# Kernel tuning notes

Hardware: AMD Instinct MI355X
Metric: run time of the kernel (lower is better)

Reference implementation:

```python
import jax, jax.numpy as jnp
import numpy as np

HIDDEN = 128
M_DIM = 128
N_NODES = 50000
N_EDGES = 600000

def _linear_params(key, fan_in, fan_out):
    k1, k2 = jax.random.split(key)
    bound = 1.0 / np.sqrt(fan_in)
    W = jax.random.uniform(k1, (fan_in, fan_out), jnp.float32, -bound, bound)
    b = jax.random.uniform(k2, (fan_out,), jnp.float32, -bound, bound)
    return W, b

def setup_inputs() -> dict:
    key = jax.random.key(0)
    ks = jax.random.split(key, 10)
    h = jax.random.normal(ks[0], (N_NODES, HIDDEN), jnp.float32)
    x = jax.random.normal(ks[1], (N_NODES, 3), jnp.float32)
    edge_index = jax.random.randint(ks[2], (2, N_EDGES), 0, N_NODES, jnp.int64)
    We1, be1 = _linear_params(ks[3], 2 * HIDDEN + 1, M_DIM)
    We2, be2 = _linear_params(ks[4], M_DIM, M_DIM)
    Wg, bg = _linear_params(ks[5], M_DIM, 1)
    Wn1, bn1 = _linear_params(ks[6], HIDDEN + M_DIM, HIDDEN)
    Wn2, bn2 = _linear_params(ks[7], HIDDEN, HIDDEN)
    Wc1, bc1 = _linear_params(ks[8], M_DIM, M_DIM)
    Wc2, bc2 = _linear_params(ks[9], M_DIM, 1)
    return {"h": h, "x": x, "edge_index": edge_index,
            "We1": We1, "be1": be1, "We2": We2, "be2": be2,
            "Wg": Wg, "bg": bg,
            "Wn1": Wn1, "bn1": bn1, "Wn2": Wn2, "bn2": bn2,
            "Wc1": Wc1, "bc1": bc1, "Wc2": Wc2, "bc2": bc2}

def reference(h, x, edge_index, We1, be1, We2, be2, Wg, bg,
              Wn1, bn1, Wn2, bn2, Wc1, bc1, Wc2, bc2):
    silu = jax.nn.silu
    row, col = edge_index[0], edge_index[1]
    N = h.shape[0]
    # gather endpoints
    x_j = x[row]          # [E, 3]
    x_i = x[col]          # [E, 3]
    coord_diff = x_i - x_j
    dist = jnp.linalg.norm(coord_diff, axis=-1, keepdims=True)  # [E, 1]
    h_j = h[row]          # [E, H]
    h_i = h[col]          # [E, H]
    msg_inputs = jnp.concatenate([h_i, h_j, dist], axis=-1)     # [E, 2H+1]
    # edge MLP: Linear -> SiLU -> Linear -> SiLU
    m_ij = silu(silu(msg_inputs @ We1 + be1) @ We2 + be2)       # [E, M]
    gate = jax.nn.sigmoid(m_ij @ Wg + bg)                       # [E, 1]
    m_ij = m_ij * gate
    # scatter-add aggregation over destination nodes
    m_aggr = jax.ops.segment_sum(m_ij, col, num_segments=N)     # [N, M]
    node_input = jnp.concatenate([h, m_aggr], axis=-1)          # [N, H+M]
    delta_h = silu(node_input @ Wn1 + bn1) @ Wn2 + bn2
    h_out = h + delta_h
    # coordinate update
    coor_weights = (silu(m_ij @ Wc1 + bc1) @ Wc2 + bc2)         # [E, 1]
    coord_updates = coord_diff * coor_weights                   # [E, 3]
    coord_aggr = jax.ops.segment_sum(coord_updates, col, num_segments=N)
    x_out = x + coord_aggr
    return (h_out, x_out)
```

## Files before the change

### kernel.cpp

```cpp
#include <hip/hip_runtime.h>
#include <cmath>

#define HID 128

typedef __attribute__((ext_vector_type(8))) short bf16x8;
typedef __attribute__((ext_vector_type(4))) float f32x4;

__device__ __forceinline__ unsigned short f2bf(float f) {
    union { float f; unsigned int i; } c; c.f = f;
    unsigned int r = c.i + 0x7fffu + ((c.i >> 16) & 1u);
    return (unsigned short)(r >> 16);
}
__device__ __forceinline__ unsigned cvt_pk(float lo, float hi) {
    unsigned r;
    asm("v_cvt_pk_bf16_f32 %0, %1, %2" : "=v"(r) : "v"(lo), "v"(hi));
    return r;
}
__device__ __forceinline__ float silu_f(float v) {
    float t = __builtin_amdgcn_exp2f(-1.44269504f * v);
    return v * __builtin_amdgcn_rcpf(1.0f + t);
}
__device__ __forceinline__ float sigmoid_f(float v) {
    return __builtin_amdgcn_rcpf(1.0f + __builtin_amdgcn_exp2f(-1.44269504f * v));
}
typedef __fp16 fp16x2 __attribute__((ext_vector_type(2)));
__device__ __forceinline__ void atomic_pk_add_f16(void* p, float lo, float hi) {
    union { fp16x2 h; unsigned u; } cv;
    cv.h = __builtin_amdgcn_cvt_pkrtz(lo, hi);
    unsigned long long a = (unsigned long long)p;
    asm volatile("global_atomic_pk_add_f16 %0, %1, off" :: "v"(a), "v"(cv.u) : "memory");
}

__global__ __launch_bounds__(256) void egnn_prep(
    const float* __restrict__ We1, const float* __restrict__ We2,
    const float* __restrict__ Wc1, const float* __restrict__ Wn1,
    const float* __restrict__ Wn2,
    short* __restrict__ We1p, short* __restrict__ We2p, short* __restrict__ Wc1p,
    short* __restrict__ Wn1p, short* __restrict__ Wn2p)
{
    int t = blockIdx.x * 256 + threadIdx.x;
    int frag = t >> 6, lane = t & 63;
    if (frag >= 224) return;
    const float* W; short* dst; int KC, f;
    if (frag < 64)       { W = We1; dst = We1p; KC = 8; f = frag; }
    else if (frag < 96)  { W = We2; dst = We2p; KC = 4; f = frag - 64; }
    else if (frag < 128) { W = Wc1; dst = Wc1p; KC = 4; f = frag - 96; }
    else if (frag < 192) { W = Wn1; dst = Wn1p; KC = 8; f = frag - 128; }
    else                 { W = Wn2; dst = Wn2p; KC = 4; f = frag - 192; }
    int nt = f / KC, kc = f % KC;
    int n = nt * 16 + (lane & 15);
    short* d = dst + (((size_t)nt * KC + kc) * 64 + lane) * 8;
    #pragma unroll
    for (int j = 0; j < 8; ++j) {
        int k = kc * 32 + ((lane >> 4) << 2) + (j & 3) + ((j >> 2) << 4);
        d[j] = (short)f2bf(W[(size_t)k * HID + n]);
    }
}

__global__ __launch_bounds__(256) void egnn_hpack(
    const float* __restrict__ h, short* __restrict__ h16, int N)
{
    int t = blockIdx.x * 256 + threadIdx.x;
    if (t < N * 32) {
        float4 v = *(const float4*)(h + (size_t)t * 4);
        uint2 p; p.x = cvt_pk(v.x, v.y); p.y = cvt_pk(v.z, v.w);
        *(uint2*)(h16 + (size_t)t * 4) = p;
    }
}

__global__ __launch_bounds__(256) void egnn_edge_mfma(
    const short* __restrict__ h16, const float* __restrict__ x,
    const int* __restrict__ ei, int E,
    const short* __restrict__ We1p, const float* __restrict__ We1,
    const float* __restrict__ be1,
    const short* __restrict__ We2p, const float* __restrict__ be2,
    const float* __restrict__ Wg, const float* __restrict__ bg,
    const short* __restrict__ Wc1p, const float* __restrict__ bc1,
    const float* __restrict__ Wc2, const float* __restrict__ bc2,
    short* __restrict__ m16, float* __restrict__ coord_aggr)
{
    __shared__ short sStage[64 * 256];
    __shared__ float s_be1[128], s_w256[128], s_be2[128];
    __shared__ float s_wg[128], s_bc1[128], s_wc2[128];
    __shared__ int   s_col[64], s_row[64];

    const int tid  = threadIdx.x;
    const int lane = tid & 63;
    const int w    = tid >> 6;
    const int l15  = lane & 15;
    const int g    = lane >> 4;
    const int e0   = blockIdx.x * 64;

    if (tid < 64) {
        s_row[tid] = ei[e0 + tid];
        s_col[tid] = ei[E + e0 + tid];
    }
    if (tid < 128) {
        s_be1[tid]  = be1[tid];
        s_w256[tid] = We1[(size_t)256 * HID + tid];
        s_be2[tid]  = be2[tid];
        s_wg[tid]   = Wg[tid];
        s_bc1[tid]  = bc1[tid];
        s_wc2[tid]  = Wc2[tid];
    }
    __syncthreads();

    #pragma unroll
    for (int it = 0; it < 16; ++it) {
        int e = w + 4 * it;
        int q = lane;
        int node = (q < 32) ? s_col[e] : s_row[e];
        uint2 v = *(const uint2*)(h16 + (size_t)node * HID + (size_t)(q & 31) * 4);
        *(uint2*)((char*)sStage + e * 512 + ((q * 8) ^ ((e & 7) << 4))) = v;
    }

    const int eloc = w * 16 + l15;
    const int nr = s_row[eloc], nc = s_col[eloc];
    float dx = x[nc * 3 + 0] - x[nr * 3 + 0];
    float dy = x[nc * 3 + 1] - x[nr * 3 + 1];
    float dz = x[nc * 3 + 2] - x[nr * 3 + 2];
    float dist = sqrtf(dx * dx + dy * dy + dz * dz);
    __syncthreads();

    const char* stageRow = (const char*)sStage + eloc * 512;
    const int sw = (eloc & 7) << 4;
    const bf16x8* A1 = (const bf16x8*)We1p;
    const bf16x8* A2 = (const bf16x8*)We2p;
    const bf16x8* A3 = (const bf16x8*)Wc1p;

    f32x4 acc[8];
    #pragma unroll
    for (int mt = 0; mt < 8; ++mt) {
        int f = mt * 16 + g * 4;
        #pragma unroll
        for (int r = 0; r < 4; ++r)
            acc[mt][r] = s_be1[f + r] + dist * s_w256[f + r];
    }
    #pragma unroll
    for (int kc = 0; kc < 8; ++kc) {
        int kb = kc * 64 + g * 8;
        uint2 lo = *(const uint2*)(stageRow + ((kb     ) ^ sw));
        uint2 hi = *(const uint2*)(stageRow + ((kb + 32) ^ sw));
        bf16x8 b; ((uint2*)&b)[0] = lo; ((uint2*)&b)[1] = hi;
        #pragma unroll
        for (int mt = 0; mt < 8; ++mt)
            acc[mt] = __builtin_amdgcn_mfma_f32_16x16x32_bf16(A1[(mt * 8 + kc) * 64 + lane], b, acc[mt], 0, 0, 0);
    }

    bf16x8 Bn[4];
    #pragma unroll
    for (int kc = 0; kc < 4; ++kc) {
        unsigned* d = (unsigned*)&Bn[kc];
        d[0] = cvt_pk(silu_f(acc[2 * kc][0]),     silu_f(acc[2 * kc][1]));
        d[1] = cvt_pk(silu_f(acc[2 * kc][2]),     silu_f(acc[2 * kc][3]));
        d[2] = cvt_pk(silu_f(acc[2 * kc + 1][0]), silu_f(acc[2 * kc + 1][1]));
        d[3] = cvt_pk(silu_f(acc[2 * kc + 1][2]), silu_f(acc[2 * kc + 1][3]));
    }

    f32x4 acc2[8];
    #pragma unroll
    for (int mt = 0; mt < 8; ++mt) {
        int f = mt * 16 + g * 4;
        #pragma unroll
        for (int r = 0; r < 4; ++r) acc2[mt][r] = s_be2[f + r];
    }
    #pragma unroll
    for (int kc = 0; kc < 4; ++kc)
        #pragma unroll
        for (int mt = 0; mt < 8; ++mt)
            acc2[mt] = __builtin_amdgcn_mfma_f32_16x16x32_bf16(A2[(mt * 4 + kc) * 64 + lane], Bn[kc], acc2[mt], 0, 0, 0);

    float gp = 0.f;
    #pragma unroll
    for (int mt = 0; mt < 8; ++mt) {
        int f = mt * 16 + g * 4;
        #pragma unroll
        for (int r = 0; r < 4; ++r) {
            float sv = silu_f(acc2[mt][r]);
            acc2[mt][r] = sv;
            gp += sv * s_wg[f + r];
        }
    }
    gp += __shfl_xor(gp, 16, 64);
    gp += __shfl_xor(gp, 32, 64);
    float gate = sigmoid_f(gp + bg[0]);

    #pragma unroll
    for (int mt = 0; mt < 8; ++mt) {
        f32x4 v;
        #pragma unroll
        for (int r = 0; r < 4; ++r) { acc2[mt][r] *= gate; v[r] = acc2[mt][r]; }
        *(f32x4*)((char*)sStage + eloc * 512 + ((g * 16 + mt * 64) ^ sw)) = v;
    }

    bf16x8 B3[4];
    #pragma unroll
    for (int kc = 0; kc < 4; ++kc) {
        unsigned* d = (unsigned*)&B3[kc];
        d[0] = cvt_pk(acc2[2 * kc][0],     acc2[2 * kc][1]);
        d[1] = cvt_pk(acc2[2 * kc][2],     acc2[2 * kc][3]);
        d[2] = cvt_pk(acc2[2 * kc + 1][0], acc2[2 * kc + 1][1]);
        d[3] = cvt_pk(acc2[2 * kc + 1][2], acc2[2 * kc + 1][3]);
    }

    #pragma unroll
    for (int i = 0; i < 16; ++i) {
        int e = w * 16 + i;
        int c = s_col[e];
        int swE = (e & 7) << 4;
        float2 v = *(const float2*)((const char*)sStage + e * 512 + ((lane * 8) ^ swE));
        atomic_pk_add_f16(m16 + (size_t)c * HID + lane * 2, v.x, v.y);
    }

    f32x4 acc3[8];
    #pragma unroll
    for (int mt = 0; mt < 8; ++mt) {
        int f = mt * 16 + g * 4;
        #pragma unroll
        for (int r = 0; r < 4; ++r) acc3[mt][r] = s_bc1[f + r];
    }
    #pragma unroll
    for (int kc = 0; kc < 4; ++kc)
        #pragma unroll
        for (int mt = 0; mt < 8; ++mt)
            acc3[mt] = __builtin_amdgcn_mfma_f32_16x16x32_bf16(A3[(mt * 4 + kc) * 64 + lane], B3[kc], acc3[mt], 0, 0, 0);

    float cwp = 0.f;
    #pragma unroll
    for (int mt = 0; mt < 8; ++mt) {
        int f = mt * 16 + g * 4;
        #pragma unroll
        for (int r = 0; r < 4; ++r)
            cwp += silu_f(acc3[mt][r]) * s_wc2[f + r];
    }
    cwp += __shfl_xor(cwp, 16, 64);
    cwp += __shfl_xor(cwp, 32, 64);
    float cw = cwp + bc2[0];
    if (g == 0) {
        atomicAdd(&coord_aggr[nc * 3 + 0], dx * cw);
        atomicAdd(&coord_aggr[nc * 3 + 1], dy * cw);
        atomicAdd(&coord_aggr[nc * 3 + 2], dz * cw);
    }
}

__global__ __launch_bounds__(256) void egnn_node_mfma(
    const float* __restrict__ h, const float* __restrict__ x,
    const short* __restrict__ m16, const float* __restrict__ coord_aggr,
    const short* __restrict__ Wn1p, const float* __restrict__ bn1,
    const short* __restrict__ Wn2p, const float* __restrict__ bn2,
    float* __restrict__ h_out, float* __restrict__ x_out, int N)
{
    __shared__ short sStage[64 * 256];
    __shared__ float s_bn1[128], s_bn2[128];

    const int tid  = threadIdx.x;
    const int lane = tid & 63;
    const int w    = tid >> 6;
    const int l15  = lane & 15;
    const int g    = lane >> 4;
    const int n0   = blockIdx.x * 64;

    if (tid < 128) { s_bn1[tid] = bn1[tid]; s_bn2[tid] = bn2[tid]; }

    if (tid < 192) {
        int gi = n0 * 3 + tid;
        if (gi < 3 * N) x_out[gi] = x[gi] + coord_aggr[gi];
    }

    #pragma unroll
    for (int it = 0; it < 16; ++it) {
        int e = w + 4 * it;
        int q = lane;
        int node = min(n0 + e, N - 1);
        uint2 pk;
        if (q < 32) {
            float4 v = *(const float4*)&h[(size_t)node * HID + (size_t)q * 4];
            pk.x = cvt_pk(v.x, v.y);
            pk.y = cvt_pk(v.z, v.w);
        } else {
            uint2 hv = *(const uint2*)((const char*)m16 + (size_t)node * 256 + (size_t)(q & 31) * 8);
            const __fp16* hp = (const __fp16*)&hv;
            pk.x = cvt_pk((float)hp[0], (float)hp[1]);
            pk.y = cvt_pk((float)hp[2], (float)hp[3]);
        }
        *(uint2*)((char*)sStage + e * 512 + ((q * 8) ^ ((e & 7) << 4))) = pk;
    }
    __syncthreads();

    const int nloc = w * 16 + l15;
    const int node = n0 + nloc;
    const char* stageRow = (const char*)sStage + nloc * 512;
    const int sw = (nloc & 7) << 4;
    const bf16x8* A1 = (const bf16x8*)Wn1p;
    const bf16x8* A2 = (const bf16x8*)Wn2p;

    f32x4 acc[8];
    #pragma unroll
    for (int mt = 0; mt < 8; ++mt) {
        int f = mt * 16 + g * 4;
        #pragma unroll
        for (int r = 0; r < 4; ++r) acc[mt][r] = s_bn1[f + r];
    }
    #pragma unroll
    for (int kc = 0; kc < 8; ++kc) {
        int kb = kc * 64 + g * 8;
        uint2 lo = *(const uint2*)(stageRow + ((kb     ) ^ sw));
        uint2 hi = *(const uint2*)(stageRow + ((kb + 32) ^ sw));
        bf16x8 b; ((uint2*)&b)[0] = lo; ((uint2*)&b)[1] = hi;
        #pragma unroll
        for (int mt = 0; mt < 8; ++mt)
            acc[mt] = __builtin_amdgcn_mfma_f32_16x16x32_bf16(A1[(mt * 8 + kc) * 64 + lane], b, acc[mt], 0, 0, 0);
    }

    bf16x8 Bn[4];
    #pragma unroll
    for (int kc = 0; kc < 4; ++kc) {
        unsigned* d = (unsigned*)&Bn[kc];
        d[0] = cvt_pk(silu_f(acc[2 * kc][0]),     silu_f(acc[2 * kc][1]));
        d[1] = cvt_pk(silu_f(acc[2 * kc][2]),     silu_f(acc[2 * kc][3]));
        d[2] = cvt_pk(silu_f(acc[2 * kc + 1][0]), silu_f(acc[2 * kc + 1][1]));
        d[3] = cvt_pk(silu_f(acc[2 * kc + 1][2]), silu_f(acc[2 * kc + 1][3]));
    }

    f32x4 acc2[8];
    #pragma unroll
    for (int mt = 0; mt < 8; ++mt) {
        int f = mt * 16 + g * 4;
        #pragma unroll
        for (int r = 0; r < 4; ++r) acc2[mt][r] = s_bn2[f + r];
    }
    #pragma unroll
    for (int kc = 0; kc < 4; ++kc)
        #pragma unroll
        for (int mt = 0; mt < 8; ++mt)
            acc2[mt] = __builtin_amdgcn_mfma_f32_16x16x32_bf16(A2[(mt * 4 + kc) * 64 + lane], Bn[kc], acc2[mt], 0, 0, 0);

    if (node < N) {
        #pragma unroll
        for (int mt = 0; mt < 8; ++mt) {
            size_t base = (size_t)node * HID + mt * 16 + g * 4;
            float4 hres = *(const float4*)&h[base];
            float4 o;
            o.x = acc2[mt][0] + hres.x;
            o.y = acc2[mt][1] + hres.y;
            o.z = acc2[mt][2] + hres.z;
            o.w = acc2[mt][3] + hres.w;
            *(float4*)&h_out[base] = o;
        }
    }
}

extern "C" void kernel_launch(void* const* d_in, const int* in_sizes, int n_in,
                              void* d_out, int out_size, void* d_ws, size_t ws_size,
                              hipStream_t stream) {
    const float* h   = (const float*)d_in[0];
    const float* x   = (const float*)d_in[1];
    const int*   ei  = (const int*)d_in[2];
    const float* We1 = (const float*)d_in[3];
    const float* be1 = (const float*)d_in[4];
    const float* We2 = (const float*)d_in[5];
    const float* be2 = (const float*)d_in[6];
    const float* Wg  = (const float*)d_in[7];
    const float* bg  = (const float*)d_in[8];
    const float* Wn1 = (const float*)d_in[9];
    const float* bn1 = (const float*)d_in[10];
    const float* Wn2 = (const float*)d_in[11];
    const float* bn2 = (const float*)d_in[12];
    const float* Wc1 = (const float*)d_in[13];
    const float* bc1 = (const float*)d_in[14];
    const float* Wc2 = (const float*)d_in[15];
    const float* bc2 = (const float*)d_in[16];

    const int N = in_sizes[0] / HID;
    const int E = in_sizes[2] / 2;

    char* p = (char*)d_ws;
    short* m16        = (short*)p;  p += (size_t)N * 256;
    float* coord_aggr = (float*)p;  p += (size_t)N * 12;
    short* h16        = (short*)p;  p += (size_t)N * 256;
    short* We1p       = (short*)p;  p += 256 * 128 * 2;
    short* We2p       = (short*)p;  p += 128 * 128 * 2;
    short* Wc1p       = (short*)p;  p += 128 * 128 * 2;
    short* Wn1p       = (short*)p;  p += 256 * 128 * 2;
    short* Wn2p       = (short*)p;  p += 128 * 128 * 2;

    (void)hipMemsetAsync(d_ws, 0, (size_t)N * 268, stream);

    float* h_out = (float*)d_out;
    float* x_out = h_out + (size_t)N * HID;

    egnn_prep<<<dim3(56), dim3(256), 0, stream>>>(
        We1, We2, Wc1, Wn1, Wn2, We1p, We2p, Wc1p, Wn1p, Wn2p);
    egnn_hpack<<<dim3((N * 32 + 255) / 256), dim3(256), 0, stream>>>(h, h16, N);
    egnn_edge_mfma<<<dim3((E + 63) / 64), dim3(256), 0, stream>>>(
        h16, x, ei, E, We1p, We1, be1, We2p, be2, Wg, bg, Wc1p, bc1, Wc2, bc2,
        m16, coord_aggr);
    egnn_node_mfma<<<dim3((N + 63) / 64), dim3(256), 0, stream>>>(
        h, x, m16, coord_aggr, Wn1p, bn1, Wn2p, bn2, h_out, x_out, N);
}
```

Before: 378.9 us.

## Split edge MLP into halves and stage messages as packed fp16 in LDS

Each of the three per-edge GEMMs now accumulates 4 output tiles at a time, in two halves, instead of all 8 at once. This roughly halves the live f32 accumulator registers and should allow higher occupancy. The post-SiLU activations are kept as bf16, gated after the reduction, and written to LDS as packed fp16 instead of fp32, so the atomic scatter reads 4-byte words. The trade-offs are extra bf16 rounding of m_ij before gating and scattering, and fewer MFMAs in flight per k-step.

```diff
diff --git a/kernel.cpp b/kernel.cpp
--- a/kernel.cpp
+++ b/kernel.cpp
@@ -16,6 +16,12 @@
     asm("v_cvt_pk_bf16_f32 %0, %1, %2" : "=v"(r) : "v"(lo), "v"(hi));
     return r;
 }
+__device__ __forceinline__ float bflo(unsigned u) {
+    union { unsigned i; float f; } c; c.i = u << 16; return c.f;
+}
+__device__ __forceinline__ float bfhi(unsigned u) {
+    union { unsigned i; float f; } c; c.i = u & 0xffff0000u; return c.f;
+}
 __device__ __forceinline__ float silu_f(float v) {
     float t = __builtin_amdgcn_exp2f(-1.44269504f * v);
     return v * __builtin_amdgcn_rcpf(1.0f + t);
@@ -24,11 +30,14 @@
     return __builtin_amdgcn_rcpf(1.0f + __builtin_amdgcn_exp2f(-1.44269504f * v));
 }
 typedef __fp16 fp16x2 __attribute__((ext_vector_type(2)));
-__device__ __forceinline__ void atomic_pk_add_f16(void* p, float lo, float hi) {
+__device__ __forceinline__ unsigned pkrtz(float lo, float hi) {
     union { fp16x2 h; unsigned u; } cv;
     cv.h = __builtin_amdgcn_cvt_pkrtz(lo, hi);
+    return cv.u;
+}
+__device__ __forceinline__ void atomic_pk_add_f16_raw(void* p, unsigned u) {
     unsigned long long a = (unsigned long long)p;
-    asm volatile("global_atomic_pk_add_f16 %0, %1, off" :: "v"(a), "v"(cv.u) : "memory");
+    asm volatile("global_atomic_pk_add_f16 %0, %1, off" :: "v"(a), "v"(u) : "memory");
 }
 
 __global__ __launch_bounds__(256) void egnn_prep(
@@ -128,79 +137,90 @@
     const bf16x8* A2 = (const bf16x8*)We2p;
     const bf16x8* A3 = (const bf16x8*)Wc1p;
 
-    f32x4 acc[8];
-    #pragma unroll
-    for (int mt = 0; mt < 8; ++mt) {
-        int f = mt * 16 + g * 4;
-        #pragma unroll
-        for (int r = 0; r < 4; ++r)
-            acc[mt][r] = s_be1[f + r] + dist * s_w256[f + r];
-    }
-    #pragma unroll
-    for (int kc = 0; kc < 8; ++kc) {
-        int kb = kc * 64 + g * 8;
-        uint2 lo = *(const uint2*)(stageRow + ((kb     ) ^ sw));
-        uint2 hi = *(const uint2*)(stageRow + ((kb + 32) ^ sw));
-        bf16x8 b; ((uint2*)&b)[0] = lo; ((uint2*)&b)[1] = hi;
-        #pragma unroll
-        for (int mt = 0; mt < 8; ++mt)
-            acc[mt] = __builtin_amdgcn_mfma_f32_16x16x32_bf16(A1[(mt * 8 + kc) * 64 + lane], b, acc[mt], 0, 0, 0);
-    }
-
     bf16x8 Bn[4];
     #pragma unroll
-    for (int kc = 0; kc < 4; ++kc) {
-        unsigned* d = (unsigned*)&Bn[kc];
-        d[0] = cvt_pk(silu_f(acc[2 * kc][0]),     silu_f(acc[2 * kc][1]));
-        d[1] = cvt_pk(silu_f(acc[2 * kc][2]),     silu_f(acc[2 * kc][3]));
-        d[2] = cvt_pk(silu_f(acc[2 * kc + 1][0]), silu_f(acc[2 * kc + 1][1]));
-        d[3] = cvt_pk(silu_f(acc[2 * kc + 1][2]), silu_f(acc[2 * kc + 1][3]));
-    }
-
-    f32x4 acc2[8];
-    #pragma unroll
-    for (int mt = 0; mt < 8; ++mt) {
-        int f = mt * 16 + g * 4;
-        #pragma unroll
-        for (int r = 0; r < 4; ++r) acc2[mt][r] = s_be2[f + r];
-    }
-    #pragma unroll
-    for (int kc = 0; kc < 4; ++kc)
-        #pragma unroll
-        for (int mt = 0; mt < 8; ++mt)
-            acc2[mt] = __builtin_amdgcn_mfma_f32_16x16x32_bf16(A2[(mt * 4 + kc) * 64 + lane], Bn[kc], acc2[mt], 0, 0, 0);
-
+    for (int half = 0; half < 2; ++half) {
+        f32x4 acc[4];
+        #pragma unroll
+        for (int m = 0; m < 4; ++m) {
+            int f = (half * 4 + m) * 16 + g * 4;
+            #pragma unroll
+            for (int r = 0; r < 4; ++r)
+                acc[m][r] = s_be1[f + r] + dist * s_w256[f + r];
+        }
+        #pragma unroll
+        for (int kc = 0; kc < 8; ++kc) {
+            int kb = kc * 64 + g * 8;
+            uint2 lo = *(const uint2*)(stageRow + ((kb     ) ^ sw));
+            uint2 hi = *(const uint2*)(stageRow + ((kb + 32) ^ sw));
+            bf16x8 b; ((uint2*)&b)[0] = lo; ((uint2*)&b)[1] = hi;
+            #pragma unroll
+            for (int m = 0; m < 4; ++m)
+                acc[m] = __builtin_amdgcn_mfma_f32_16x16x32_bf16(
+                    A1[((half * 4 + m) * 8 + kc) * 64 + lane], b, acc[m], 0, 0, 0);
+        }
+        #pragma unroll
+        for (int p = 0; p < 2; ++p) {
+            unsigned* d = (unsigned*)&Bn[half * 2 + p];
+            d[0] = cvt_pk(silu_f(acc[2 * p][0]),     silu_f(acc[2 * p][1]));
+            d[1] = cvt_pk(silu_f(acc[2 * p][2]),     silu_f(acc[2 * p][3]));
+            d[2] = cvt_pk(silu_f(acc[2 * p + 1][0]), silu_f(acc[2 * p + 1][1]));
+            d[3] = cvt_pk(silu_f(acc[2 * p + 1][2]), silu_f(acc[2 * p + 1][3]));
+        }
+    }
+
+    bf16x8 Pn[4];
     float gp = 0.f;
     #pragma unroll
-    for (int mt = 0; mt < 8; ++mt) {
-        int f = mt * 16 + g * 4;
-        #pragma unroll
-        for (int r = 0; r < 4; ++r) {
-            float sv = silu_f(acc2[mt][r]);
-            acc2[mt][r] = sv;
-            gp += sv * s_wg[f + r];
+    for (int half = 0; half < 2; ++half) {
+        f32x4 acc[4];
+        #pragma unroll
+        for (int m = 0; m < 4; ++m) {
+            int f = (half * 4 + m) * 16 + g * 4;
+            #pragma unroll
+            for (int r = 0; r < 4; ++r) acc[m][r] = s_be2[f + r];
+        }
+        #pragma unroll
+        for (int kc = 0; kc < 4; ++kc)
+            #pragma unroll
+            for (int m = 0; m < 4; ++m)
+                acc[m] = __builtin_amdgcn_mfma_f32_16x16x32_bf16(
+                    A2[((half * 4 + m) * 4 + kc) * 64 + lane], Bn[kc], acc[m], 0, 0, 0);
+        #pragma unroll
+        for (int m = 0; m < 4; ++m) {
+            int f = (half * 4 + m) * 16 + g * 4;
+            #pragma unroll
+            for (int r = 0; r < 4; ++r) {
+                float sv = silu_f(acc[m][r]);
+                acc[m][r] = sv;
+                gp += sv * s_wg[f + r];
+            }
+        }
+        #pragma unroll
+        for (int p = 0; p < 2; ++p) {
+            unsigned* d = (unsigned*)&Pn[half * 2 + p];
+            d[0] = cvt_pk(acc[2 * p][0],     acc[2 * p][1]);
+            d[1] = cvt_pk(acc[2 * p][2],     acc[2 * p][3]);
+            d[2] = cvt_pk(acc[2 * p + 1][0], acc[2 * p + 1][1]);
+            d[3] = cvt_pk(acc[2 * p + 1][2], acc[2 * p + 1][3]);
         }
     }
     gp += __shfl_xor(gp, 16, 64);
     gp += __shfl_xor(gp, 32, 64);
     float gate = sigmoid_f(gp + bg[0]);
 
-    #pragma unroll
-    for (int mt = 0; mt < 8; ++mt) {
-        f32x4 v;
-        #pragma unroll
-        for (int r = 0; r < 4; ++r) { acc2[mt][r] *= gate; v[r] = acc2[mt][r]; }
-        *(f32x4*)((char*)sStage + eloc * 512 + ((g * 16 + mt * 64) ^ sw)) = v;
-    }
-
     bf16x8 B3[4];
     #pragma unroll
     for (int kc = 0; kc < 4; ++kc) {
+        const unsigned* s = (const unsigned*)&Pn[kc];
         unsigned* d = (unsigned*)&B3[kc];
-        d[0] = cvt_pk(acc2[2 * kc][0],     acc2[2 * kc][1]);
-        d[1] = cvt_pk(acc2[2 * kc][2],     acc2[2 * kc][3]);
-        d[2] = cvt_pk(acc2[2 * kc + 1][0], acc2[2 * kc + 1][1]);
-        d[3] = cvt_pk(acc2[2 * kc + 1][2], acc2[2 * kc + 1][3]);
+        uint2 w0, w1;
+        { float lo = bflo(s[0]) * gate, hi = bfhi(s[0]) * gate; d[0] = cvt_pk(lo, hi); w0.x = pkrtz(lo, hi); }
+        { float lo = bflo(s[1]) * gate, hi = bfhi(s[1]) * gate; d[1] = cvt_pk(lo, hi); w0.y = pkrtz(lo, hi); }
+        { float lo = bflo(s[2]) * gate, hi = bfhi(s[2]) * gate; d[2] = cvt_pk(lo, hi); w1.x = pkrtz(lo, hi); }
+        { float lo = bflo(s[3]) * gate, hi = bfhi(s[3]) * gate; d[3] = cvt_pk(lo, hi); w1.y = pkrtz(lo, hi); }
+        *(uint2*)((char*)sStage + eloc * 512 + (((2 * kc) * 32 + g * 8) ^ sw))     = w0;
+        *(uint2*)((char*)sStage + eloc * 512 + (((2 * kc + 1) * 32 + g * 8) ^ sw)) = w1;
     }
 
     #pragma unroll
@@ -208,30 +228,33 @@
         int e = w * 16 + i;
         int c = s_col[e];
         int swE = (e & 7) << 4;
-        float2 v = *(const float2*)((const char*)sStage + e * 512 + ((lane * 8) ^ swE));
-        atomic_pk_add_f16(m16 + (size_t)c * HID + lane * 2, v.x, v.y);
-    }
-
-    f32x4 acc3[8];
-    #pragma unroll
-    for (int mt = 0; mt < 8; ++mt) {
-        int f = mt * 16 + g * 4;
-        #pragma unroll
-        for (int r = 0; r < 4; ++r) acc3[mt][r] = s_bc1[f + r];
-    }
-    #pragma unroll
-    for (int kc = 0; kc < 4; ++kc)
-        #pragma unroll
-        for (int mt = 0; mt < 8; ++mt)
-            acc3[mt] = __builtin_amdgcn_mfma_f32_16x16x32_bf16(A3[(mt * 4 + kc) * 64 + lane], B3[kc], acc3[mt], 0, 0, 0);
+        unsigned v = *(const unsigned*)((const char*)sStage + e * 512 + ((lane * 4) ^ swE));
+        atomic_pk_add_f16_raw(m16 + (size_t)c * HID + lane * 2, v);
+    }
 
     float cwp = 0.f;
     #pragma unroll
-    for (int mt = 0; mt < 8; ++mt) {
-        int f = mt * 16 + g * 4;
-        #pragma unroll
-        for (int r = 0; r < 4; ++r)
-            cwp += silu_f(acc3[mt][r]) * s_wc2[f + r];
+    for (int half = 0; half < 2; ++half) {
+        f32x4 acc[4];
+        #pragma unroll
+        for (int m = 0; m < 4; ++m) {
+            int f = (half * 4 + m) * 16 + g * 4;
+            #pragma unroll
+            for (int r = 0; r < 4; ++r) acc[m][r] = s_bc1[f + r];
+        }
+        #pragma unroll
+        for (int kc = 0; kc < 4; ++kc)
+            #pragma unroll
+            for (int m = 0; m < 4; ++m)
+                acc[m] = __builtin_amdgcn_mfma_f32_16x16x32_bf16(
+                    A3[((half * 4 + m) * 4 + kc) * 64 + lane], B3[kc], acc[m], 0, 0, 0);
+        #pragma unroll
+        for (int m = 0; m < 4; ++m) {
+            int f = (half * 4 + m) * 16 + g * 4;
+            #pragma unroll
+            for (int r = 0; r < 4; ++r)
+                cwp += silu_f(acc[m][r]) * s_wc2[f + r];
+        }
     }
     cwp += __shfl_xor(cwp, 16, 64);
     cwp += __shfl_xor(cwp, 32, 64);
```

Measured after the change: 587.8 us. 1.55x slower.
